# Kernel optimization log

Measured on AMD Instinct MI355X. Metric: run time of the kernel, lower is better.

Reference implementation:

```python
import jax, jax.numpy as jnp
import numpy as np

N_NEURONS = 256
P_MAX = 8
N_BLOCKS = P_MAX + 1
HIDDEN = 32
BATCH = 8192


def setup_inputs() -> dict:
    key = jax.random.key(0)
    ks = jax.random.split(key, 9)
    z = jax.random.normal(ks[0], (BATCH, N_BLOCKS * N_NEURONS), dtype=jnp.float32)
    # Per-block ScalarMLP params, stacked over the n_blocks axis.
    s1 = 1.0 / np.sqrt(N_NEURONS)
    s2 = 1.0 / np.sqrt(HIDDEN)
    gW1 = jax.random.uniform(ks[1], (N_BLOCKS, N_NEURONS, HIDDEN), jnp.float32, -s1, s1)
    gb1 = jax.random.uniform(ks[2], (N_BLOCKS, HIDDEN), jnp.float32, -s1, s1)
    gW2 = jax.random.uniform(ks[3], (N_BLOCKS, HIDDEN, HIDDEN), jnp.float32, -s2, s2)
    gb2 = jax.random.uniform(ks[4], (N_BLOCKS, HIDDEN), jnp.float32, -s2, s2)
    gW3 = jax.random.uniform(ks[5], (N_BLOCKS, HIDDEN), jnp.float32, -s2, s2)
    gb3 = jax.random.uniform(ks[6], (N_BLOCKS,), jnp.float32, -s2, s2)
    # Lag coupling matrices W_r ~ U(-init_scale, init_scale), init_scale=0.1
    W = jax.random.uniform(ks[7], (P_MAX, N_NEURONS, N_NEURONS), jnp.float32, -0.1, 0.1)
    return {"z": z, "gW1": gW1, "gb1": gb1, "gW2": gW2, "gb2": gb2,
            "gW3": gW3, "gb3": gb3, "W": W}


def _energy(z, gW1, gb1, gW2, gb2, gW3, gb3, W):
    B = z.shape[0]
    blocks = z.reshape(B, N_BLOCKS, N_NEURONS)           # (B, K, n)
    # Per-block ScalarMLP energies (all blocks at once).
    h1 = jax.nn.silu(jnp.einsum('bkn,knh->bkh', blocks, gW1) + gb1)   # (B, K, H)
    h2 = jax.nn.silu(jnp.einsum('bkh,khg->bkg', h1, gW2) + gb2)       # (B, K, H)
    e = jnp.einsum('bkh,kh->bk', h2, gW3) + gb3                        # (B, K)
    # Bilinear lag couplings: z_future^T W_r z_{lag-r}, r = 1..p_max.
    z_future = blocks[:, P_MAX, :]                                     # (B, n)
    lags = blocks[:, :P_MAX, :][:, ::-1, :]                            # (B, p, n), index r-1 == block p_max-r
    cross = jnp.einsum('bi,rij,brj->b', z_future, W, lags)             # (B,)
    return e.sum(axis=-1) + cross                                      # (B,)


def reference(z, gW1, gb1, gW2, gb2, gW3, gb3, W):
    # Score s(z) = -grad_z U(z); sum over batch gives per-sample grads
    # since energies are independent across samples.
    grad_z = jax.grad(lambda zz: _energy(zz, gW1, gb1, gW2, gb2, gW3, gb3, W).sum())(z)
    return -grad_z
```

## Files before the change

kernel.cpp:

```cpp
#include <hip/hip_runtime.h>
#include <hip/hip_bf16.h>
#include <math.h>

#define BATCH 8192
#define NB 9
#define NN 256
#define PMAX 8
#define HID 32
#define ZDIM 2304

typedef short bf16x8 __attribute__((ext_vector_type(8)));
typedef float f32x4 __attribute__((ext_vector_type(4)));

static __device__ inline unsigned short f2bf(float f) {
    __hip_bfloat16 h = __float2bfloat16(f);
    return *reinterpret_cast<unsigned short*>(&h);
}

static __device__ inline uint4 pack8(float4 a, float4 b) {
    uint4 u;
    u.x = (unsigned)f2bf(a.x) | ((unsigned)f2bf(a.y) << 16);
    u.y = (unsigned)f2bf(a.z) | ((unsigned)f2bf(a.w) << 16);
    u.z = (unsigned)f2bf(b.x) | ((unsigned)f2bf(b.y) << 16);
    u.w = (unsigned)f2bf(b.z) | ((unsigned)f2bf(b.w) << 16);
    return u;
}

__global__ __launch_bounds__(256) void k_pack(
    const float* __restrict__ W, const float* __restrict__ gW1,
    unsigned short* __restrict__ Wf, unsigned short* __restrict__ WTb,
    unsigned short* __restrict__ gW1b, unsigned short* __restrict__ g1Tb) {
    int r = blockIdx.z;
    int t = threadIdx.x;
    if (r < 8) {
        __shared__ float tt[32][33];
        int i0 = blockIdx.y * 32;
        int j0 = blockIdx.x * 32;
        int tx = t & 31;
        int ty = t >> 5;
        const float* src = W + (size_t)r * 65536;
        int kc2b = ((7 - r) << 3) + (j0 >> 5);
        int j = j0 + tx;
        #pragma unroll
        for (int s = 0; s < 32; s += 8) {
            int i = i0 + ty + s;
            float v = src[(size_t)i * 256 + j];
            tt[ty + s][tx] = v;
            size_t widx = ((size_t)(kc2b * 16 + (i >> 4)) * 64
                           + ((i & 15) + 16 * ((j >> 3) & 3))) * 8 + (j & 7);
            Wf[widx] = f2bf(v);
        }
        __syncthreads();
        #pragma unroll
        for (int s = 0; s < 32; s += 8)
            WTb[(size_t)r * 65536 + (size_t)(j0 + ty + s) * 256 + (i0 + tx)] = f2bf(tt[tx][ty + s]);
    } else {
        int tg = (blockIdx.y * 8 + blockIdx.x) * 256 + t;
        for (int e = tg; e < 73728; e += 16384) {
            float v = gW1[e];
            unsigned short b = f2bf(v);
            gW1b[e] = b;
            int k = e >> 13, n = (e >> 5) & 255, h = e & 31;
            g1Tb[(size_t)(k * 32 + h) * 256 + n] = b;
        }
    }
}

__global__ __launch_bounds__(256) void k_mlp(
    const float* __restrict__ z, const unsigned short* __restrict__ g1Tb,
    const float* __restrict__ gb1, const float* __restrict__ gW2,
    const float* __restrict__ gb2, const float* __restrict__ gW3,
    unsigned short* __restrict__ d1f, unsigned short* __restrict__ zf) {
    __shared__ uint4 As4[2][256];
    __shared__ uint4 Bw[1024];
    __shared__ uint4 W2Ts4[128];
    __shared__ uint4 W2Ns4[128];

    int t = threadIdx.x;
    int lane = t & 63;
    int w = t >> 6;
    int k = blockIdx.y;
    int b0 = blockIdx.x * 64;
    uint4* zfu = (uint4*)zf;
    uint4* d1fu = (uint4*)d1f;
    int rb0 = b0 >> 4;

    const unsigned short* bsrc = g1Tb + (size_t)k * 8192;
    for (int e = t; e < 1024; e += 256) {
        int h = e >> 5;
        int rest = e & 31;
        int c = rest >> 2, qq = rest & 3;
        Bw[c * 128 + (h & 15) + 16 * qq + 64 * (h >> 4)] =
            *(const uint4*)(bsrc + (size_t)h * 256 + c * 32 + qq * 8);
    }
    const float* gw2 = gW2 + (size_t)k * 1024;
    unsigned short* w2t = (unsigned short*)W2Ts4;
    unsigned short* w2n = (unsigned short*)W2Ns4;
    for (int e = t; e < 1024; e += 256) {
        int n = e >> 5, kk = e & 31;
        int qq = kk >> 3, jj = kk & 7;
        int ci = (n & 15) + 16 * qq + 64 * (n >> 4);
        w2t[ci * 8 + jj] = f2bf(gw2[kk * 32 + n]);
        w2n[ci * 8 + jj] = f2bf(gw2[n * 32 + kk]);
    }

    int mq = t >> 2;
    int q = t & 3;
    int ci0 = (mq & 15) + 16 * q + 64 * (mq >> 4);

    f32x4 acc1[2];
    #pragma unroll
    for (int j = 0; j < 2; ++j) acc1[j] = (f32x4){0.f, 0.f, 0.f, 0.f};

    auto loadZ = [&](int c, float4 (&fa)[2]) {
        const float* as = z + (size_t)(b0 + mq) * ZDIM + k * 256 + c * 32 + q * 8;
        fa[0] = *(const float4*)(as);
        fa[1] = *(const float4*)(as + 4);
    };
    auto sinkZ = [&](int buf, int c, float4 (&fa)[2]) {
        uint4 pk = pack8(fa[0], fa[1]);
        As4[buf][ci0] = pk;
        zfu[((size_t)(rb0 + (ci0 >> 6)) * 72 + (k * 8 + c)) * 64 + (ci0 & 63)] = pk;
    };

    {
        float4 fa[2];
        loadZ(0, fa);
        sinkZ(0, 0, fa);
    }
    int cur = 0;
    for (int c = 0; c < 8; ++c) {
        __syncthreads();
        float4 fan[2];
        if (c < 7) loadZ(c + 1, fan);
        bf16x8 af = __builtin_bit_cast(bf16x8, As4[cur][w * 64 + lane]);
        bf16x8 bfr[2];
        #pragma unroll
        for (int j = 0; j < 2; ++j) bfr[j] = __builtin_bit_cast(bf16x8, Bw[c * 128 + lane + j * 64]);
        #pragma unroll
        for (int j = 0; j < 2; ++j)
            acc1[j] = __builtin_amdgcn_mfma_f32_16x16x32_bf16(af, bfr[j], acc1[j], 0, 0, 0);
        if (c < 7) sinkZ(cur ^ 1, c + 1, fan);
        cur ^= 1;
    }

    int cq = lane >> 4;
    int ci16 = lane & 15;
    float b1v[2], b2v[2], g3v[2];
    #pragma unroll
    for (int j = 0; j < 2; ++j) {
        b1v[j] = gb1[k * 32 + j * 16 + ci16];
        b2v[j] = gb2[k * 32 + j * 16 + ci16];
        g3v[j] = gW3[k * 32 + j * 16 + ci16];
    }
    unsigned short* Hs = (unsigned short*)As4;
    float sp1[2][4];
    __syncthreads();
    #pragma unroll
    for (int j = 0; j < 2; ++j)
        #pragma unroll
        for (int r = 0; r < 4; ++r) {
            float a1 = acc1[j][r] + b1v[j];
            float s1 = 1.f / (1.f + __expf(-a1));
            sp1[j][r] = s1 * (1.f + a1 * (1.f - s1));
            int col = j * 16 + ci16;
            int chunk = ci16 + 16 * (col >> 3) + 64 * w;
            chunk = (cq * 4 + r) + 16 * (col >> 3) + 64 * w;
            Hs[chunk * 8 + (col & 7)] = f2bf(a1 * s1);
        }
    __syncthreads();

    bf16x8 af2 = __builtin_bit_cast(bf16x8, As4[0][w * 64 + lane]);
    bf16x8 wf[2];
    #pragma unroll
    for (int j = 0; j < 2; ++j) wf[j] = __builtin_bit_cast(bf16x8, W2Ts4[lane + j * 64]);
    f32x4 acc2[2];
    #pragma unroll
    for (int j = 0; j < 2; ++j) {
        acc2[j] = (f32x4){0.f, 0.f, 0.f, 0.f};
        acc2[j] = __builtin_amdgcn_mfma_f32_16x16x32_bf16(af2, wf[j], acc2[j], 0, 0, 0);
    }

    __syncthreads();
    #pragma unroll
    for (int j = 0; j < 2; ++j)
        #pragma unroll
        for (int r = 0; r < 4; ++r) {
            float a2 = acc2[j][r] + b2v[j];
            float s2 = 1.f / (1.f + __expf(-a2));
            float da2 = g3v[j] * s2 * (1.f + a2 * (1.f - s2));
            int col = j * 16 + ci16;
            int chunk = (cq * 4 + r) + 16 * (col >> 3) + 64 * w;
            Hs[chunk * 8 + (col & 7)] = f2bf(da2);
        }
    __syncthreads();

    bf16x8 af3 = __builtin_bit_cast(bf16x8, As4[0][w * 64 + lane]);
    bf16x8 wg[2];
    #pragma unroll
    for (int j = 0; j < 2; ++j) wg[j] = __builtin_bit_cast(bf16x8, W2Ns4[lane + j * 64]);
    __syncthreads();
    #pragma unroll
    for (int j = 0; j < 2; ++j) {
        f32x4 a3 = (f32x4){0.f, 0.f, 0.f, 0.f};
        a3 = __builtin_amdgcn_mfma_f32_16x16x32_bf16(af3, wg[j], a3, 0, 0, 0);
        #pragma unroll
        for (int r = 0; r < 4; ++r) {
            int col = j * 16 + ci16;
            int chunk = (cq * 4 + r) + 16 * (col >> 3) + 64 * w;
            Hs[chunk * 8 + (col & 7)] = f2bf(a3[r] * sp1[j][r]);
        }
    }
    __syncthreads();
    d1fu[((size_t)k * 512 + rb0 + (t >> 6)) * 64 + (t & 63)] = As4[0][t];
}

__global__ __launch_bounds__(256) void k_gemm_lo(
    const unsigned short* __restrict__ zf, const unsigned short* __restrict__ d1f,
    const unsigned short* __restrict__ WTb, const unsigned short* __restrict__ gW1b,
    float* __restrict__ out) {
    __shared__ uint4 As4[2][512];
    __shared__ uint4 Bs4[2][512];

    int t = threadIdx.x;
    int lane = t & 63;
    int w = t >> 6;
    int wr = w >> 1, wc = w & 1;
    int b0 = blockIdx.x * 128;
    int n0 = blockIdx.y * 128;
    int k  = n0 >> 8;
    int jb = n0 & 255;

    const uint4* zfu  = (const uint4*)zf;
    const uint4* d1fu = (const uint4*)d1f;
    int rb0 = b0 >> 4;
    const unsigned short* Bmain = WTb + (size_t)(7 - k) * 65536 + (size_t)jb * 256;
    const unsigned short* Bext  = gW1b + ((size_t)k * 256 + jb) * 32;

    int mq = t >> 2;
    int q  = t & 3;
    int ci0 = (mq & 15) + 16 * q + 64 * (mq >> 4);

    auto loadAB = [&](int c, uint4 (&au)[2], uint4 (&bu)[2]) {
        #pragma unroll
        for (int pp = 0; pp < 2; ++pp) {
            int m = mq + 64 * pp;
            int ci = ci0 + 256 * pp;
            if (c < 8) {
                au[pp] = zfu[((size_t)(rb0 + (ci >> 6)) * 72 + 64 + c) * 64 + (ci & 63)];
                bu[pp] = *(const uint4*)(Bmain + (size_t)m * 256 + c * 32 + q * 8);
            } else {
                au[pp] = d1fu[((size_t)k * 512 + rb0 + (ci >> 6)) * 64 + (ci & 63)];
                bu[pp] = *(const uint4*)(Bext + (size_t)m * 32 + q * 8);
            }
        }
    };
    auto storeAB = [&](int buf, uint4 (&au)[2], uint4 (&bu)[2]) {
        #pragma unroll
        for (int pp = 0; pp < 2; ++pp) {
            int idx = ci0 + 256 * pp;
            As4[buf][idx] = au[pp];
            Bs4[buf][idx] = bu[pp];
        }
    };

    f32x4 acc[4][4];
    #pragma unroll
    for (int i = 0; i < 4; ++i)
        #pragma unroll
        for (int j = 0; j < 4; ++j) acc[i][j] = (f32x4){0.f, 0.f, 0.f, 0.f};

    {
        uint4 au[2], bu[2];
        loadAB(0, au, bu);
        storeAB(0, au, bu);
    }
    int cur = 0;
    for (int c = 0; c < 9; ++c) {
        __syncthreads();
        uint4 aun[2], bun[2];
        if (c < 8) loadAB(c + 1, aun, bun);
        bf16x8 af[4], bf[4];
        #pragma unroll
        for (int i = 0; i < 4; ++i) af[i] = __builtin_bit_cast(bf16x8, As4[cur][lane + (wr * 4 + i) * 64]);
        #pragma unroll
        for (int j = 0; j < 4; ++j) bf[j] = __builtin_bit_cast(bf16x8, Bs4[cur][lane + (wc * 4 + j) * 64]);
        #pragma unroll
        for (int i = 0; i < 4; ++i)
            #pragma unroll
            for (int j = 0; j < 4; ++j)
                acc[i][j] = __builtin_amdgcn_mfma_f32_16x16x32_bf16(af[i], bf[j], acc[i][j], 0, 0, 0);
        if (c < 8) storeAB(cur ^ 1, aun, bun);
        cur ^= 1;
    }

    int rquad = lane >> 4;
    int cidx  = lane & 15;
    #pragma unroll
    for (int i = 0; i < 4; ++i) {
        #pragma unroll
        for (int j = 0; j < 4; ++j) {
            float* o = out + (size_t)(b0 + wr * 64 + i * 16 + rquad * 4) * ZDIM
                     + (k * 256 + jb + wc * 64 + j * 16 + cidx);
            #pragma unroll
            for (int r = 0; r < 4; ++r)
                o[(size_t)r * ZDIM] = -acc[i][j][r];
        }
    }
}

__global__ __launch_bounds__(256) void k_gemm_hi(
    const unsigned short* __restrict__ zf, const unsigned short* __restrict__ d1f,
    const unsigned short* __restrict__ Wf, const unsigned short* __restrict__ gW1b,
    float* __restrict__ out) {
    int t = threadIdx.x;
    int lane = t & 63;
    int w = t >> 6;
    int b0 = blockIdx.x * 64;
    int i0 = blockIdx.y * 64;

    int rl = lane & 15;
    int kq = lane >> 4;

    int rb = (b0 >> 4) + w;
    const uint4* Abase = (const uint4*)zf + (size_t)rb * 72 * 64 + lane;
    const uint4* Atail = (const uint4*)d1f + ((size_t)8 * 512 + rb) * 64 + lane;
    const uint4* Bbase = (const uint4*)Wf + (size_t)(i0 >> 4) * 64 + lane;

    f32x4 acc[4];
    #pragma unroll
    for (int j = 0; j < 4; ++j) acc[j] = (f32x4){0.f, 0.f, 0.f, 0.f};

    auto loadA = [&](int c, uint4& x) {
        x = (c < 64) ? Abase[(size_t)c * 64] : Atail[0];
    };
    auto loadB = [&](int c, uint4 (&bb)[4]) {
        if (c < 64) {
            #pragma unroll
            for (int j = 0; j < 4; ++j)
                bb[j] = Bbase[(size_t)c * 1024 + j * 64];
        } else {
            #pragma unroll
            for (int j = 0; j < 4; ++j)
                bb[j] = *(const uint4*)(gW1b + (size_t)(8 * 256 + i0 + j * 16 + rl) * 32 + kq * 8);
        }
    };

    uint4 a;
    uint4 bb[4];
    loadA(0, a);
    loadB(0, bb);
    for (int c = 0; c < 65; ++c) {
        uint4 na;
        uint4 nbb[4];
        if (c < 64) {
            loadA(c + 1, na);
            loadB(c + 1, nbb);
        }
        bf16x8 af = __builtin_bit_cast(bf16x8, a);
        #pragma unroll
        for (int j = 0; j < 4; ++j)
            acc[j] = __builtin_amdgcn_mfma_f32_16x16x32_bf16(
                af, __builtin_bit_cast(bf16x8, bb[j]), acc[j], 0, 0, 0);
        if (c < 64) {
            a = na;
            #pragma unroll
            for (int j = 0; j < 4; ++j) bb[j] = nbb[j];
        }
    }

    #pragma unroll
    for (int j = 0; j < 4; ++j) {
        float* o = out + (size_t)(b0 + w * 16 + kq * 4) * ZDIM + 2048 + i0 + j * 16 + rl;
        #pragma unroll
        for (int r = 0; r < 4; ++r)
            o[(size_t)r * ZDIM] = -acc[j][r];
    }
}

extern "C" void kernel_launch(void* const* d_in, const int* in_sizes, int n_in,
                              void* d_out, int out_size, void* d_ws, size_t ws_size,
                              hipStream_t stream) {
    const float* z   = (const float*)d_in[0];
    const float* gW1 = (const float*)d_in[1];
    const float* gb1 = (const float*)d_in[2];
    const float* gW2 = (const float*)d_in[3];
    const float* gb2 = (const float*)d_in[4];
    const float* gW3 = (const float*)d_in[5];
    const float* W   = (const float*)d_in[7];
    float* out = (float*)d_out;

    unsigned short* d1f  = (unsigned short*)d_ws;
    unsigned short* WTb  = d1f + 2359296;
    unsigned short* Wf   = WTb + 524288;
    unsigned short* gW1b = Wf + 524288;
    unsigned short* g1Tb = gW1b + 73728;
    unsigned short* zf   = g1Tb + 73728;

    k_pack<<<dim3(8, 8, 9), 256, 0, stream>>>(W, gW1, Wf, WTb, gW1b, g1Tb);
    k_mlp<<<dim3(128, 9), 256, 0, stream>>>(z, g1Tb, gb1, gW2, gb2, gW3, d1f, zf);
    k_gemm_lo<<<dim3(64, 16), 256, 0, stream>>>(zf, d1f, WTb, gW1b, out);
    k_gemm_hi<<<dim3(128, 4), 256, 0, stream>>>(zf, d1f, Wf, gW1b, out);
}
```

Measured before the change: 203.1 us.

## Pre-swizzle W transpose for MFMA, drop LDS in gemm_lo, deepen prefetch

k_pack now writes the transposed W directly in MFMA fragment-swizzled order, which removes the shared-memory transpose. k_gemm_lo is rewritten to stream A and B fragments straight from global memory with no LDS staging, using a 64x64 tile and a 3-deep register prefetch. k_gemm_hi gets the same 3-stage unrolled prefetch, and k_mlp loads all eight z chunks up front so the per-chunk barriers go away. The goal is to hide global load latency and cut synchronisation, at the cost of more registers and less data reuse per block in gemm_lo.

```diff
diff --git a/kernel.cpp b/kernel.cpp
--- a/kernel.cpp
+++ b/kernel.cpp
@@ -28,12 +28,11 @@
 
 __global__ __launch_bounds__(256) void k_pack(
     const float* __restrict__ W, const float* __restrict__ gW1,
-    unsigned short* __restrict__ Wf, unsigned short* __restrict__ WTb,
+    unsigned short* __restrict__ Wf, unsigned short* __restrict__ WTf,
     unsigned short* __restrict__ gW1b, unsigned short* __restrict__ g1Tb) {
     int r = blockIdx.z;
     int t = threadIdx.x;
     if (r < 8) {
-        __shared__ float tt[32][33];
         int i0 = blockIdx.y * 32;
         int j0 = blockIdx.x * 32;
         int tx = t & 31;
@@ -45,15 +44,14 @@
         for (int s = 0; s < 32; s += 8) {
             int i = i0 + ty + s;
             float v = src[(size_t)i * 256 + j];
-            tt[ty + s][tx] = v;
+            unsigned short b = f2bf(v);
             size_t widx = ((size_t)(kc2b * 16 + (i >> 4)) * 64
                            + ((i & 15) + 16 * ((j >> 3) & 3))) * 8 + (j & 7);
-            Wf[widx] = f2bf(v);
-        }
-        __syncthreads();
-        #pragma unroll
-        for (int s = 0; s < 32; s += 8)
-            WTb[(size_t)r * 65536 + (size_t)(j0 + ty + s) * 256 + (i0 + tx)] = f2bf(tt[tx][ty + s]);
+            Wf[widx] = b;
+            size_t tidx = ((size_t)(((7 - r) * 8 + (i >> 5)) * 16 + (j >> 4)) * 64
+                           + ((j & 15) + 16 * ((i >> 3) & 3))) * 8 + (i & 7);
+            WTf[tidx] = b;
+        }
     } else {
         int tg = (blockIdx.y * 8 + blockIdx.x) * 256 + t;
         for (int e = tg; e < 73728; e += 16384) {
@@ -71,7 +69,7 @@
     const float* __restrict__ gb1, const float* __restrict__ gW2,
     const float* __restrict__ gb2, const float* __restrict__ gW3,
     unsigned short* __restrict__ d1f, unsigned short* __restrict__ zf) {
-    __shared__ uint4 As4[2][256];
+    __shared__ uint4 Az[8][256];
     __shared__ uint4 Bw[1024];
     __shared__ uint4 W2Ts4[128];
     __shared__ uint4 W2Ns4[128];
@@ -84,6 +82,18 @@
     uint4* zfu = (uint4*)zf;
     uint4* d1fu = (uint4*)d1f;
     int rb0 = b0 >> 4;
+
+    int mq = t >> 2;
+    int q = t & 3;
+    int ci0 = (mq & 15) + 16 * q + 64 * (mq >> 4);
+
+    float4 fa[8][2];
+    #pragma unroll
+    for (int c = 0; c < 8; ++c) {
+        const float* as = z + (size_t)(b0 + mq) * ZDIM + k * 256 + c * 32 + q * 8;
+        fa[c][0] = *(const float4*)(as);
+        fa[c][1] = *(const float4*)(as + 4);
+    }
 
     const unsigned short* bsrc = g1Tb + (size_t)k * 8192;
     for (int e = t; e < 1024; e += 256) {
@@ -104,44 +114,24 @@
         w2n[ci * 8 + jj] = f2bf(gw2[n * 32 + kk]);
     }
 
-    int mq = t >> 2;
-    int q = t & 3;
-    int ci0 = (mq & 15) + 16 * q + 64 * (mq >> 4);
+    #pragma unroll
+    for (int c = 0; c < 8; ++c) {
+        uint4 pk = pack8(fa[c][0], fa[c][1]);
+        Az[c][ci0] = pk;
+        zfu[((size_t)(rb0 + (ci0 >> 6)) * 72 + (k * 8 + c)) * 64 + (ci0 & 63)] = pk;
+    }
+    __syncthreads();
 
     f32x4 acc1[2];
     #pragma unroll
     for (int j = 0; j < 2; ++j) acc1[j] = (f32x4){0.f, 0.f, 0.f, 0.f};
-
-    auto loadZ = [&](int c, float4 (&fa)[2]) {
-        const float* as = z + (size_t)(b0 + mq) * ZDIM + k * 256 + c * 32 + q * 8;
-        fa[0] = *(const float4*)(as);
-        fa[1] = *(const float4*)(as + 4);
-    };
-    auto sinkZ = [&](int buf, int c, float4 (&fa)[2]) {
-        uint4 pk = pack8(fa[0], fa[1]);
-        As4[buf][ci0] = pk;
-        zfu[((size_t)(rb0 + (ci0 >> 6)) * 72 + (k * 8 + c)) * 64 + (ci0 & 63)] = pk;
-    };
-
-    {
-        float4 fa[2];
-        loadZ(0, fa);
-        sinkZ(0, 0, fa);
-    }
-    int cur = 0;
+    #pragma unroll
     for (int c = 0; c < 8; ++c) {
-        __syncthreads();
-        float4 fan[2];
-        if (c < 7) loadZ(c + 1, fan);
-        bf16x8 af = __builtin_bit_cast(bf16x8, As4[cur][w * 64 + lane]);
-        bf16x8 bfr[2];
-        #pragma unroll
-        for (int j = 0; j < 2; ++j) bfr[j] = __builtin_bit_cast(bf16x8, Bw[c * 128 + lane + j * 64]);
+        bf16x8 af = __builtin_bit_cast(bf16x8, Az[c][w * 64 + lane]);
         #pragma unroll
         for (int j = 0; j < 2; ++j)
-            acc1[j] = __builtin_amdgcn_mfma_f32_16x16x32_bf16(af, bfr[j], acc1[j], 0, 0, 0);
-        if (c < 7) sinkZ(cur ^ 1, c + 1, fan);
-        cur ^= 1;
+            acc1[j] = __builtin_amdgcn_mfma_f32_16x16x32_bf16(
+                af, __builtin_bit_cast(bf16x8, Bw[c * 128 + lane + j * 64]), acc1[j], 0, 0, 0);
     }
 
     int cq = lane >> 4;
@@ -153,7 +143,7 @@
         b2v[j] = gb2[k * 32 + j * 16 + ci16];
         g3v[j] = gW3[k * 32 + j * 16 + ci16];
     }
-    unsigned short* Hs = (unsigned short*)As4;
+    unsigned short* Hs = (unsigned short*)Az;
     float sp1[2][4];
     __syncthreads();
     #pragma unroll
@@ -164,21 +154,18 @@
             float s1 = 1.f / (1.f + __expf(-a1));
             sp1[j][r] = s1 * (1.f + a1 * (1.f - s1));
             int col = j * 16 + ci16;
-            int chunk = ci16 + 16 * (col >> 3) + 64 * w;
-            chunk = (cq * 4 + r) + 16 * (col >> 3) + 64 * w;
+            int chunk = (cq * 4 + r) + 16 * (col >> 3) + 64 * w;
             Hs[chunk * 8 + (col & 7)] = f2bf(a1 * s1);
         }
     __syncthreads();
 
-    bf16x8 af2 = __builtin_bit_cast(bf16x8, As4[0][w * 64 + lane]);
-    bf16x8 wf[2];
-    #pragma unroll
-    for (int j = 0; j < 2; ++j) wf[j] = __builtin_bit_cast(bf16x8, W2Ts4[lane + j * 64]);
+    bf16x8 af2 = __builtin_bit_cast(bf16x8, Az[0][w * 64 + lane]);
     f32x4 acc2[2];
     #pragma unroll
     for (int j = 0; j < 2; ++j) {
         acc2[j] = (f32x4){0.f, 0.f, 0.f, 0.f};
-        acc2[j] = __builtin_amdgcn_mfma_f32_16x16x32_bf16(af2, wf[j], acc2[j], 0, 0, 0);
+        acc2[j] = __builtin_amdgcn_mfma_f32_16x16x32_bf16(
+            af2, __builtin_bit_cast(bf16x8, W2Ts4[lane + j * 64]), acc2[j], 0, 0, 0);
     }
 
     __syncthreads();
@@ -195,15 +182,13 @@
         }
     __syncthreads();
 
-    bf16x8 af3 = __builtin_bit_cast(bf16x8, As4[0][w * 64 + lane]);
-    bf16x8 wg[2];
-    #pragma unroll
-    for (int j = 0; j < 2; ++j) wg[j] = __builtin_bit_cast(bf16x8, W2Ns4[lane + j * 64]);
+    bf16x8 af3 = __builtin_bit_cast(bf16x8, Az[0][w * 64 + lane]);
     __syncthreads();
     #pragma unroll
     for (int j = 0; j < 2; ++j) {
         f32x4 a3 = (f32x4){0.f, 0.f, 0.f, 0.f};
-        a3 = __builtin_amdgcn_mfma_f32_16x16x32_bf16(af3, wg[j], a3, 0, 0, 0);
+        a3 = __builtin_amdgcn_mfma_f32_16x16x32_bf16(
+            af3, __builtin_bit_cast(bf16x8, W2Ns4[lane + j * 64]), a3, 0, 0, 0);
         #pragma unroll
         for (int r = 0; r < 4; ++r) {
             int col = j * 16 + ci16;
@@ -212,100 +197,82 @@
         }
     }
     __syncthreads();
-    d1fu[((size_t)k * 512 + rb0 + (t >> 6)) * 64 + (t & 63)] = As4[0][t];
+    d1fu[((size_t)k * 512 + rb0 + (t >> 6)) * 64 + (t & 63)] = Az[0][t];
 }
 
 __global__ __launch_bounds__(256) void k_gemm_lo(
     const unsigned short* __restrict__ zf, const unsigned short* __restrict__ d1f,
-    const unsigned short* __restrict__ WTb, const unsigned short* __restrict__ gW1b,
+    const unsigned short* __restrict__ WTf, const unsigned short* __restrict__ gW1b,
     float* __restrict__ out) {
-    __shared__ uint4 As4[2][512];
-    __shared__ uint4 Bs4[2][512];
-
     int t = threadIdx.x;
     int lane = t & 63;
     int w = t >> 6;
-    int wr = w >> 1, wc = w & 1;
-    int b0 = blockIdx.x * 128;
-    int n0 = blockIdx.y * 128;
-    int k  = n0 >> 8;
-    int jb = n0 & 255;
-
-    const uint4* zfu  = (const uint4*)zf;
-    const uint4* d1fu = (const uint4*)d1f;
-    int rb0 = b0 >> 4;
-    const unsigned short* Bmain = WTb + (size_t)(7 - k) * 65536 + (size_t)jb * 256;
-    const unsigned short* Bext  = gW1b + ((size_t)k * 256 + jb) * 32;
-
-    int mq = t >> 2;
-    int q  = t & 3;
-    int ci0 = (mq & 15) + 16 * q + 64 * (mq >> 4);
-
-    auto loadAB = [&](int c, uint4 (&au)[2], uint4 (&bu)[2]) {
-        #pragma unroll
-        for (int pp = 0; pp < 2; ++pp) {
-            int m = mq + 64 * pp;
-            int ci = ci0 + 256 * pp;
-            if (c < 8) {
-                au[pp] = zfu[((size_t)(rb0 + (ci >> 6)) * 72 + 64 + c) * 64 + (ci & 63)];
-                bu[pp] = *(const uint4*)(Bmain + (size_t)m * 256 + c * 32 + q * 8);
-            } else {
-                au[pp] = d1fu[((size_t)k * 512 + rb0 + (ci >> 6)) * 64 + (ci & 63)];
-                bu[pp] = *(const uint4*)(Bext + (size_t)m * 32 + q * 8);
-            }
-        }
-    };
-    auto storeAB = [&](int buf, uint4 (&au)[2], uint4 (&bu)[2]) {
-        #pragma unroll
-        for (int pp = 0; pp < 2; ++pp) {
-            int idx = ci0 + 256 * pp;
-            As4[buf][idx] = au[pp];
-            Bs4[buf][idx] = bu[pp];
-        }
-    };
-
-    f32x4 acc[4][4];
-    #pragma unroll
-    for (int i = 0; i < 4; ++i)
-        #pragma unroll
-        for (int j = 0; j < 4; ++j) acc[i][j] = (f32x4){0.f, 0.f, 0.f, 0.f};
-
-    {
-        uint4 au[2], bu[2];
-        loadAB(0, au, bu);
-        storeAB(0, au, bu);
-    }
-    int cur = 0;
-    for (int c = 0; c < 9; ++c) {
-        __syncthreads();
-        uint4 aun[2], bun[2];
-        if (c < 8) loadAB(c + 1, aun, bun);
-        bf16x8 af[4], bf[4];
-        #pragma unroll
-        for (int i = 0; i < 4; ++i) af[i] = __builtin_bit_cast(bf16x8, As4[cur][lane + (wr * 4 + i) * 64]);
-        #pragma unroll
-        for (int j = 0; j < 4; ++j) bf[j] = __builtin_bit_cast(bf16x8, Bs4[cur][lane + (wc * 4 + j) * 64]);
-        #pragma unroll
-        for (int i = 0; i < 4; ++i)
+    int b0 = blockIdx.x * 64;
+    int i0 = blockIdx.y * 64;
+    int k  = i0 >> 8;
+    int g0 = (i0 >> 4) & 15;
+    int rl = lane & 15;
+    int kq = lane >> 4;
+    int rb = (b0 >> 4) + w;
+
+    const uint4* Abase = (const uint4*)zf + ((size_t)rb * 72 + 64) * 64 + lane;
+    const uint4* Atail = (const uint4*)d1f + ((size_t)k * 512 + rb) * 64 + lane;
+    const uint4* Bbase = (const uint4*)WTf + ((size_t)(k * 8) * 16 + g0) * 64 + lane;
+    const unsigned short* Btail = gW1b + ((size_t)(k * 256) + (i0 & 255) + rl) * 32 + kq * 8;
+
+    f32x4 acc[4];
+    #pragma unroll
+    for (int j = 0; j < 4; ++j) acc[j] = (f32x4){0.f, 0.f, 0.f, 0.f};
+
+    auto loadA = [&](int c, uint4& x) {
+        x = (c < 8) ? Abase[(size_t)c * 64] : Atail[0];
+    };
+    auto loadB = [&](int c, uint4 (&bb)[4]) {
+        if (c < 8) {
             #pragma unroll
             for (int j = 0; j < 4; ++j)
-                acc[i][j] = __builtin_amdgcn_mfma_f32_16x16x32_bf16(af[i], bf[j], acc[i][j], 0, 0, 0);
-        if (c < 8) storeAB(cur ^ 1, aun, bun);
-        cur ^= 1;
-    }
-
-    int rquad = lane >> 4;
-    int cidx  = lane & 15;
-    #pragma unroll
-    for (int i = 0; i < 4; ++i) {
-        #pragma unroll
-        for (int j = 0; j < 4; ++j) {
-            float* o = out + (size_t)(b0 + wr * 64 + i * 16 + rquad * 4) * ZDIM
-                     + (k * 256 + jb + wc * 64 + j * 16 + cidx);
-            #pragma unroll
-            for (int r = 0; r < 4; ++r)
-                o[(size_t)r * ZDIM] = -acc[i][j][r];
-        }
+                bb[j] = Bbase[((size_t)c * 16 + j) * 64];
+        } else {
+            #pragma unroll
+            for (int j = 0; j < 4; ++j)
+                bb[j] = *(const uint4*)(Btail + j * 512);
+        }
+    };
+    auto doStep = [&](uint4 a, uint4 (&bb)[4]) {
+        bf16x8 af = __builtin_bit_cast(bf16x8, a);
+        #pragma unroll
+        for (int j = 0; j < 4; ++j)
+            acc[j] = __builtin_amdgcn_mfma_f32_16x16x32_bf16(
+                af, __builtin_bit_cast(bf16x8, bb[j]), acc[j], 0, 0, 0);
+    };
+
+    uint4 a0, a1, a2, b0_[4], b1_[4], b2_[4];
+    loadA(0, a0); loadB(0, b0_);
+    loadA(1, a1); loadB(1, b1_);
+    loadA(2, a2); loadB(2, b2_);
+    #pragma unroll
+    for (int base = 0; base < 9; base += 3) {
+        uint4 na0, na1, na2, nb0[4], nb1[4], nb2[4];
+        const bool pf = (base + 3) < 9;
+        if (pf) { loadA(base + 3, na0); loadB(base + 3, nb0); }
+        doStep(a0, b0_);
+        if (pf) { loadA(base + 4, na1); loadB(base + 4, nb1); }
+        doStep(a1, b1_);
+        if (pf) { loadA(base + 5, na2); loadB(base + 5, nb2); }
+        doStep(a2, b2_);
+        if (pf) {
+            a0 = na0; a1 = na1; a2 = na2;
+            #pragma unroll
+            for (int j = 0; j < 4; ++j) { b0_[j] = nb0[j]; b1_[j] = nb1[j]; b2_[j] = nb2[j]; }
+        }
+    }
+
+    #pragma unroll
+    for (int j = 0; j < 4; ++j) {
+        float* o = out + (size_t)(b0 + w * 16 + kq * 4) * ZDIM + i0 + j * 16 + rl;
+        #pragma unroll
+        for (int r = 0; r < 4; ++r)
+            o[(size_t)r * ZDIM] = -acc[j][r];
     }
 }
 
@@ -321,8 +288,8 @@
 
     int rl = lane & 15;
     int kq = lane >> 4;
-
     int rb = (b0 >> 4) + w;
+
     const uint4* Abase = (const uint4*)zf + (size_t)rb * 72 * 64 + lane;
     const uint4* Atail = (const uint4*)d1f + ((size_t)8 * 512 + rb) * 64 + lane;
     const uint4* Bbase = (const uint4*)Wf + (size_t)(i0 >> 4) * 64 + lane;
@@ -345,29 +312,38 @@
                 bb[j] = *(const uint4*)(gW1b + (size_t)(8 * 256 + i0 + j * 16 + rl) * 32 + kq * 8);
         }
     };
-
-    uint4 a;
-    uint4 bb[4];
-    loadA(0, a);
-    loadB(0, bb);
-    for (int c = 0; c < 65; ++c) {
-        uint4 na;
-        uint4 nbb[4];
-        if (c < 64) {
-            loadA(c + 1, na);
-            loadB(c + 1, nbb);
-        }
+    auto doStep = [&](uint4 a, uint4 (&bb)[4]) {
         bf16x8 af = __builtin_bit_cast(bf16x8, a);
         #pragma unroll
         for (int j = 0; j < 4; ++j)
             acc[j] = __builtin_amdgcn_mfma_f32_16x16x32_bf16(
                 af, __builtin_bit_cast(bf16x8, bb[j]), acc[j], 0, 0, 0);
-        if (c < 64) {
-            a = na;
-            #pragma unroll
-            for (int j = 0; j < 4; ++j) bb[j] = nbb[j];
-        }
-    }
+    };
+
+    uint4 a0, a1, a2, b0_[4], b1_[4], b2_[4];
+    loadA(0, a0); loadB(0, b0_);
+    loadA(1, a1); loadB(1, b1_);
+    loadA(2, a2); loadB(2, b2_);
+    for (int base = 0; base < 63; base += 3) {
+        uint4 na0, na1, na2, nb0[4], nb1[4], nb2[4];
+        loadA(base + 3, na0); loadB(base + 3, nb0);
+        doStep(a0, b0_);
+        loadA(base + 4, na1); loadB(base + 4, nb1);
+        doStep(a1, b1_);
+        bool pf2 = (base + 5) < 65;
+        if (pf2) { loadA(base + 5, na2); loadB(base + 5, nb2); }
+        doStep(a2, b2_);
+        a0 = na0; a1 = na1;
+        #pragma unroll
+        for (int j = 0; j < 4; ++j) { b0_[j] = nb0[j]; b1_[j] = nb1[j]; }
+        if (pf2) {
+            a2 = na2;
+            #pragma unroll
+            for (int j = 0; j < 4; ++j) b2_[j] = nb2[j];
+        }
+    }
+    doStep(a0, b0_);
+    doStep(a1, b1_);
 
     #pragma unroll
     for (int j = 0; j < 4; ++j) {
@@ -391,14 +367,14 @@
     float* out = (float*)d_out;
 
     unsigned short* d1f  = (unsigned short*)d_ws;
-    unsigned short* WTb  = d1f + 2359296;
-    unsigned short* Wf   = WTb + 524288;
+    unsigned short* WTf  = d1f + 2359296;
+    unsigned short* Wf   = WTf + 524288;
     unsigned short* gW1b = Wf + 524288;
     unsigned short* g1Tb = gW1b + 73728;
     unsigned short* zf   = g1Tb + 73728;
 
-    k_pack<<<dim3(8, 8, 9), 256, 0, stream>>>(W, gW1, Wf, WTb, gW1b, g1Tb);
+    k_pack<<<dim3(8, 8, 9), 256, 0, stream>>>(W, gW1, Wf, WTf, gW1b, g1Tb);
     k_mlp<<<dim3(128, 9), 256, 0, stream>>>(z, g1Tb, gb1, gW2, gb2, gW3, d1f, zf);
-    k_gemm_lo<<<dim3(64, 16), 256, 0, stream>>>(zf, d1f, WTb, gW1b, out);
+    k_gemm_lo<<<dim3(128, 32), 256, 0, stream>>>(zf, d1f, WTf, gW1b, out);
     k_gemm_hi<<<dim3(128, 4), 256, 0, stream>>>(zf, d1f, Wf, gW1b, out);
 }
```

New measurement: 204.0 us. About the same (+0.4%).
